# Kernel tuning notes

Measured on AMD Instinct MI355X. Metric: run time of the kernel, lower is better.

The kernel has to match this reference:

```python
import jax, jax.numpy as jnp
import numpy as np

N, E, F_IN, HID, HEADS, B = 50000, 800000, 128, 128, 2, 256
EPS = 1e-5
NEG_SLOPE = 0.2


def gat_conv(x, src, dst, W, a_src, a_dst, b, heads, out_c, concat):
    n = x.shape[0]
    h = (x @ W).reshape(n, heads, out_c)            # [N,H,C]
    alpha_src = jnp.sum(h * a_src, axis=-1)          # [N,H]
    alpha_dst = jnp.sum(h * a_dst, axis=-1)          # [N,H]
    e = jax.nn.leaky_relu(alpha_src[src] + alpha_dst[dst], NEG_SLOPE)  # [E2,H]
    # segment softmax over incoming edges per destination node
    emax = jax.ops.segment_max(e, dst, num_segments=n)
    ex = jnp.exp(e - emax[dst])
    denom = jax.ops.segment_sum(ex, dst, num_segments=n)
    alpha = ex / denom[dst]                          # [E2,H]
    msg = h[src] * alpha[:, :, None]                 # [E2,H,C]
    out = jax.ops.segment_sum(msg, dst, num_segments=n)  # [N,H,C]
    if concat:
        out = out.reshape(n, heads * out_c)
    else:
        out = out.mean(axis=1)
    return out + b


def batchnorm_eval(x, gamma, beta, mean, var):
    return gamma * (x - mean) * jax.lax.rsqrt(var + EPS) + beta


def setup_inputs() -> dict:
    key = jax.random.key(0)
    ks = jax.random.split(key, 16)
    x = jax.random.normal(ks[0], (N, F_IN), dtype=jnp.float32)
    edge_index = jax.random.randint(ks[1], (2, E), 0, N, dtype=jnp.int64)
    batch = (jnp.arange(N, dtype=jnp.int64) * B) // N  # sorted, every graph non-empty
    s1 = 1.0 / np.sqrt(F_IN)
    s2 = 1.0 / np.sqrt(HEADS * HID)
    return {
        "x": x,
        "edge_index": edge_index,
        "batch": batch,
        "W1": jax.random.normal(ks[2], (F_IN, HEADS * HID), dtype=jnp.float32) * s1,
        "a_src1": jax.random.normal(ks[3], (HEADS, HID), dtype=jnp.float32) * s1,
        "a_dst1": jax.random.normal(ks[4], (HEADS, HID), dtype=jnp.float32) * s1,
        "b1": jnp.zeros((HEADS * HID,), dtype=jnp.float32),
        "gamma1": jnp.ones((HEADS * HID,), dtype=jnp.float32),
        "beta1": jnp.zeros((HEADS * HID,), dtype=jnp.float32),
        "rm1": jax.random.normal(ks[5], (HEADS * HID,), dtype=jnp.float32) * 0.1,
        "rv1": jax.random.uniform(ks[6], (HEADS * HID,), dtype=jnp.float32, minval=0.5, maxval=1.5),
        "W2": jax.random.normal(ks[7], (HEADS * HID, HID), dtype=jnp.float32) * s2,
        "a_src2": jax.random.normal(ks[8], (1, HID), dtype=jnp.float32) * s2,
        "a_dst2": jax.random.normal(ks[9], (1, HID), dtype=jnp.float32) * s2,
        "b2": jnp.zeros((HID,), dtype=jnp.float32),
        "gamma2": jnp.ones((HID,), dtype=jnp.float32),
        "beta2": jnp.zeros((HID,), dtype=jnp.float32),
        "rm2": jax.random.normal(ks[10], (HID,), dtype=jnp.float32) * 0.1,
        "rv2": jax.random.uniform(ks[11], (HID,), dtype=jnp.float32, minval=0.5, maxval=1.5),
    }


def reference(x, edge_index, batch, W1, a_src1, a_dst1, b1, gamma1, beta1, rm1, rv1,
              W2, a_src2, a_dst2, b2, gamma2, beta2, rm2, rv2):
    n = x.shape[0]
    # PyG GATConv adds self-loops by default
    loops = jnp.arange(n, dtype=edge_index.dtype)
    src = jnp.concatenate([edge_index[0], loops])
    dst = jnp.concatenate([edge_index[1], loops])

    h = gat_conv(x, src, dst, W1, a_src1, a_dst1, b1, HEADS, HID, concat=True)
    h = jax.nn.relu(batchnorm_eval(h, gamma1, beta1, rm1, rv1))  # dropout = identity (eval)

    h = gat_conv(h, src, dst, W2, a_src2, a_dst2, b2, 1, HID, concat=False)
    h = jax.nn.relu(batchnorm_eval(h, gamma2, beta2, rm2, rv2))

    # global max pool over graphs
    h_D = jax.ops.segment_max(h, batch, num_segments=B)  # [B, HID]
    return h_D
```

## Files before the change

### kernel.cpp

```cpp
#include <hip/hip_runtime.h>
#include <hip/hip_bf16.h>
#include <math.h>

#define NEG_SLOPE 0.2f
#define EPSBN 1e-5f

typedef __attribute__((ext_vector_type(8))) short bf16x8;
typedef __attribute__((ext_vector_type(4))) float f32x4;

__device__ __forceinline__ float bfu2f(unsigned u_lo16) { return __uint_as_float(u_lo16 << 16); }
__device__ __forceinline__ unsigned short f2bf(float f) {
    return __bfloat16_as_ushort(__float2bfloat16(f));
}
__device__ __forceinline__ void splitf(float v, unsigned short &h, unsigned short &l) {
    __hip_bfloat16 hb = __float2bfloat16(v);
    float r = v - __bfloat162float(hb);
    h = __bfloat16_as_ushort(hb);
    l = __bfloat16_as_ushort(__float2bfloat16(r));
}

__global__ __launch_bounds__(256) void precompute_v(
    const float* __restrict__ W1, const float* __restrict__ as1,
    const float* __restrict__ ad1, float* __restrict__ vsd)
{
    int idx = blockIdx.x * 256 + threadIdx.x;
    if (idx >= 512) return;
    int k = idx & 127, which = idx >> 7;
    const float* av = ((which >= 2) ? ad1 : as1) + ((which & 1) ? 128 : 0);
    const float* wr = W1 + (size_t)k * 256 + ((which & 1) ? 128 : 0);
    float v = 0.f;
    for (int c = 0; c < 128; ++c) v += wr[c] * av[c];
    vsd[which * 128 + k] = v;
}

__global__ __launch_bounds__(256) void prep(
    const float* __restrict__ X, const float* __restrict__ vsd,
    const float* __restrict__ W1, const float* __restrict__ W2,
    const int* __restrict__ ei,
    unsigned short* __restrict__ Xh, float* __restrict__ asrc, float* __restrict__ adst,
    unsigned short* __restrict__ w1th, unsigned short* __restrict__ w1tl,
    unsigned short* __restrict__ w2th, unsigned short* __restrict__ w2tl,
    int* __restrict__ counts, int* __restrict__ erank,
    int Nn, int E, int nwB, int countB)
{
    const int b = blockIdx.x;
    const int tid = threadIdx.x;
    if (b < nwB) {
        int n = (int)((b * 256 + tid) >> 6);
        int lane = tid & 63;
        if (n >= Nn) return;
        float2 xv = *(const float2*)(X + (size_t)n * 128 + lane * 2);
        unsigned short hh[2] = {f2bf(xv.x), f2bf(xv.y)};
        *(unsigned*)(Xh + (size_t)n * 128 + lane * 2) = *(unsigned*)hh;
        int k = lane * 2;
        float p0 = xv.x * vsd[k]       + xv.y * vsd[k + 1];
        float p1 = xv.x * vsd[128 + k] + xv.y * vsd[129 + k];
        float p2 = xv.x * vsd[256 + k] + xv.y * vsd[257 + k];
        float p3 = xv.x * vsd[384 + k] + xv.y * vsd[385 + k];
        for (int off = 32; off; off >>= 1) {
            p0 += __shfl_xor(p0, off); p1 += __shfl_xor(p1, off);
            p2 += __shfl_xor(p2, off); p3 += __shfl_xor(p3, off);
        }
        if (lane == 0) {
            asrc[n * 2] = p0; asrc[n * 2 + 1] = p1;
            adst[n * 2] = p2; adst[n * 2 + 1] = p3;
        }
    } else if (b < nwB + countB) {
        int base = (b - nwB) * 2048 + tid;
        int E2 = E + Nn;
#pragma unroll
        for (int k = 0; k < 8; ++k) {
            int e = base + k * 256;
            if (e < E2) {
                int dst = (e < E) ? ei[E + e] : (e - E);
                erank[e] = atomicAdd(&counts[dst], 1);
            }
        }
    } else {
        int idx = (b - nwB - countB) * 256 + tid;
        if (idx < 32768) {
            int nn = idx >> 7, k = idx & 127;
            unsigned short h, l; splitf(W1[(size_t)k * 256 + nn], h, l);
            w1th[idx] = h; w1tl[idx] = l;
        } else if (idx < 65536) {
            int j = idx - 32768;
            int nn = j >> 8, k = j & 255;
            unsigned short h, l; splitf(W2[(size_t)k * 128 + nn], h, l);
            w2th[j] = h; w2tl[j] = l;
        }
    }
}

__global__ __launch_bounds__(256) void scan_block(
    const int* __restrict__ counts, int* __restrict__ offs, int* __restrict__ bsum, int Nn)
{
    __shared__ int s[256];
    int i = blockIdx.x * 256 + threadIdx.x;
    int v = (i < Nn) ? counts[i] : 0;
    s[threadIdx.x] = v;
    __syncthreads();
    for (int off = 1; off < 256; off <<= 1) {
        int t = (threadIdx.x >= off) ? s[threadIdx.x - off] : 0;
        __syncthreads();
        s[threadIdx.x] += t;
        __syncthreads();
    }
    if (i < Nn) offs[i] = s[threadIdx.x] - v;
    if (threadIdx.x == 255) bsum[blockIdx.x] = s[255];
}

__global__ __launch_bounds__(256) void finalize_offsets(
    const int* __restrict__ bsum, int* __restrict__ offs, int Nn, int E2)
{
    __shared__ int ws[4];
    int b = blockIdx.x, t = threadIdx.x;
    int v = (t < b) ? bsum[t] : 0;
    for (int off = 32; off; off >>= 1) v += __shfl_xor(v, off);
    if ((t & 63) == 0) ws[t >> 6] = v;
    __syncthreads();
    int S = ws[0] + ws[1] + ws[2] + ws[3];
    int i = b * 256 + t;
    if (i < Nn) offs[i] += S;
    if (b == 0 && t == 0) offs[Nn] = E2;
}

__global__ __launch_bounds__(256) void fill_edges(
    const int* __restrict__ ei, int E, int Nn,
    const int* __restrict__ offs, const int* __restrict__ erank,
    int* __restrict__ esrc)
{
    int base = blockIdx.x * 1024 + threadIdx.x;
    int E2 = E + Nn;
#pragma unroll
    for (int k = 0; k < 4; ++k) {
        int e = base + k * 256;
        if (e >= E2) continue;
        int src, dst;
        if (e < E) { src = ei[e]; dst = ei[E + e]; }
        else       { src = e - E; dst = e - E; }
        esrc[offs[dst] + erank[e]] = src;
    }
}

__device__ __forceinline__ void fma8(float wA, uint4 hv, float acc[8])
{
    acc[0] = fmaf(wA, bfu2f(hv.x & 0xffff), acc[0]);
    acc[1] = fmaf(wA, __uint_as_float(hv.x & 0xffff0000u), acc[1]);
    acc[2] = fmaf(wA, bfu2f(hv.y & 0xffff), acc[2]);
    acc[3] = fmaf(wA, __uint_as_float(hv.y & 0xffff0000u), acc[3]);
    acc[4] = fmaf(wA, bfu2f(hv.z & 0xffff), acc[4]);
    acc[5] = fmaf(wA, __uint_as_float(hv.z & 0xffff0000u), acc[5]);
    acc[6] = fmaf(wA, bfu2f(hv.w & 0xffff), acc[6]);
    acc[7] = fmaf(wA, __uint_as_float(hv.w & 0xffff0000u), acc[7]);
}

__device__ __forceinline__ void fma8x2(float wa, float wb, uint4 hv,
                                       float a0[8], float a1[8])
{
    float f;
    f = bfu2f(hv.x & 0xffff);                 a0[0]=fmaf(wa,f,a0[0]); a1[0]=fmaf(wb,f,a1[0]);
    f = __uint_as_float(hv.x & 0xffff0000u);  a0[1]=fmaf(wa,f,a0[1]); a1[1]=fmaf(wb,f,a1[1]);
    f = bfu2f(hv.y & 0xffff);                 a0[2]=fmaf(wa,f,a0[2]); a1[2]=fmaf(wb,f,a1[2]);
    f = __uint_as_float(hv.y & 0xffff0000u);  a0[3]=fmaf(wa,f,a0[3]); a1[3]=fmaf(wb,f,a1[3]);
    f = bfu2f(hv.z & 0xffff);                 a0[4]=fmaf(wa,f,a0[4]); a1[4]=fmaf(wb,f,a1[4]);
    f = __uint_as_float(hv.z & 0xffff0000u);  a0[5]=fmaf(wa,f,a0[5]); a1[5]=fmaf(wb,f,a1[5]);
    f = bfu2f(hv.w & 0xffff);                 a0[6]=fmaf(wa,f,a0[6]); a1[6]=fmaf(wb,f,a1[6]);
    f = __uint_as_float(hv.w & 0xffff0000u);  a0[7]=fmaf(wa,f,a0[7]); a1[7]=fmaf(wb,f,a1[7]);
}

__device__ __forceinline__ void gather1h(
    int sj, float w, int nc, int sub,
    const char* __restrict__ hb_c, float acc[8])
{
    for (int t = 0; t < nc; t += 4) {
        int e = t + sub;
        int sA = __shfl(sj, e);
        float wA = __shfl(w, e);
        uint4 hv = *(const uint4*)(hb_c + sA * 256);
        fma8(wA, hv, acc);
    }
}

__device__ __forceinline__ void gatherx(
    int sj, float w0, float w1, int nc, int sub,
    const char* __restrict__ hb_c, float a0[8], float a1[8])
{
    for (int t = 0; t < nc; t += 4) {
        int e = t + sub;
        int sA = __shfl(sj, e);
        float wa = __shfl(w0, e);
        float wb = __shfl(w1, e);
        uint4 hv = *(const uint4*)(hb_c + sA * 256);
        fma8x2(wa, wb, hv, a0, a1);
    }
}

__global__ __launch_bounds__(256) void spmm_x(
    const unsigned short* __restrict__ xh, const float* __restrict__ asrc,
    const float* __restrict__ adst, const int* __restrict__ offs,
    const int* __restrict__ esrc,
    unsigned short* __restrict__ xth, int Nn)
{
    int d = (int)((blockIdx.x * blockDim.x + threadIdx.x) >> 6);
    int lane = threadIdx.x & 63;
    if (d >= Nn) return;
    int beg = offs[d], end = offs[d + 1];
    int deg = end - beg;
    float ad0 = adst[d * 2], ad1 = adst[d * 2 + 1];
    const int sub = lane >> 4;
    const int cgrp = lane & 15;
    const char* hb_c = (const char*)xh + cgrp * 16;
    float a0[8] = {}, a1[8] = {};

    if (deg <= 64) {
        int sj = 0; float e0 = -1e30f, e1 = -1e30f;
        if (lane < deg) {
            sj = esrc[beg + lane];
            float2 av = *(const float2*)(asrc + (size_t)sj * 2);
            e0 = av.x + ad0; e0 = e0 > 0.f ? e0 : NEG_SLOPE * e0;
            e1 = av.y + ad1; e1 = e1 > 0.f ? e1 : NEG_SLOPE * e1;
        }
        float m0 = e0, m1 = e1;
        for (int off = 32; off; off >>= 1) {
            m0 = fmaxf(m0, __shfl_xor(m0, off));
            m1 = fmaxf(m1, __shfl_xor(m1, off));
        }
        float p0 = (lane < deg) ? expf(e0 - m0) : 0.f;
        float p1 = (lane < deg) ? expf(e1 - m1) : 0.f;
        float s0 = p0, s1 = p1;
        for (int off = 32; off; off >>= 1) {
            s0 += __shfl_xor(s0, off);
            s1 += __shfl_xor(s1, off);
        }
        float w0 = p0 * (1.f / s0), w1 = p1 * (1.f / s1);
        gatherx(sj, w0, w1, deg, sub, hb_c, a0, a1);
    } else {
        float m0 = -1e30f, m1 = -1e30f;
        for (int j = beg + lane; j < end; j += 64) {
            int s = esrc[j];
            float2 av = *(const float2*)(asrc + (size_t)s * 2);
            float e0 = av.x + ad0; e0 = e0 > 0.f ? e0 : NEG_SLOPE * e0;
            float e1 = av.y + ad1; e1 = e1 > 0.f ? e1 : NEG_SLOPE * e1;
            m0 = fmaxf(m0, e0); m1 = fmaxf(m1, e1);
        }
        for (int off = 32; off; off >>= 1) {
            m0 = fmaxf(m0, __shfl_xor(m0, off));
            m1 = fmaxf(m1, __shfl_xor(m1, off));
        }
        float s0 = 0.f, s1 = 0.f;
        for (int j = beg + lane; j < end; j += 64) {
            int s = esrc[j];
            float2 av = *(const float2*)(asrc + (size_t)s * 2);
            float e0 = av.x + ad0; e0 = e0 > 0.f ? e0 : NEG_SLOPE * e0;
            float e1 = av.y + ad1; e1 = e1 > 0.f ? e1 : NEG_SLOPE * e1;
            s0 += expf(e0 - m0); s1 += expf(e1 - m1);
        }
        for (int off = 32; off; off >>= 1) {
            s0 += __shfl_xor(s0, off);
            s1 += __shfl_xor(s1, off);
        }
        float rd0 = 1.f / s0, rd1 = 1.f / s1;
        for (int base = beg; base < end; base += 64) {
            int nc = end - base; if (nc > 64) nc = 64;
            int sj = 0; float w0 = 0.f, w1 = 0.f;
            if (lane < nc) {
                sj = esrc[base + lane];
                float2 av = *(const float2*)(asrc + (size_t)sj * 2);
                float e0 = av.x + ad0; e0 = e0 > 0.f ? e0 : NEG_SLOPE * e0;
                float e1 = av.y + ad1; e1 = e1 > 0.f ? e1 : NEG_SLOPE * e1;
                w0 = expf(e0 - m0) * rd0;
                w1 = expf(e1 - m1) * rd1;
            }
            gatherx(sj, w0, w1, nc, sub, hb_c, a0, a1);
        }
    }
#pragma unroll
    for (int i = 0; i < 8; ++i) {
        a0[i] += __shfl_xor(a0[i], 32); a0[i] += __shfl_xor(a0[i], 16);
        a1[i] += __shfl_xor(a1[i], 32); a1[i] += __shfl_xor(a1[i], 16);
    }
    if (lane < 16) {
        int cl = cgrp * 8;
        unsigned short h0[8], h1[8];
#pragma unroll
        for (int i = 0; i < 8; ++i) { h0[i] = f2bf(a0[i]); h1[i] = f2bf(a1[i]); }
        size_t rb = (size_t)d * 256;
        *(uint4*)(xth + rb + cl)       = *(uint4*)&h0[0];
        *(uint4*)(xth + rb + 128 + cl) = *(uint4*)&h1[0];
    }
}

__global__ __launch_bounds__(256) void gemm_bn_split(
    const unsigned short* __restrict__ Ah,
    const unsigned short* __restrict__ Bth, const unsigned short* __restrict__ Btl,
    const float* __restrict__ bias, const float* __restrict__ gamma,
    const float* __restrict__ beta, const float* __restrict__ rm,
    const float* __restrict__ rv,
    unsigned short* __restrict__ Ch, int M)
{
    __shared__ unsigned short smem[3][128][32];
    const int tid = threadIdx.x;
    const int lane = tid & 63;
    const int wave = tid >> 6;
    const int fr = lane & 15, g = lane >> 4;
    const int wr = (wave >> 1) * 64, wc = (wave & 1) * 64;
    const int rowBase = blockIdx.x * 128, colBase = blockIdx.y * 128;

    f32x4 acc[4][4] = {};

    for (int kk = 0; kk < 128; kk += 32) {
#pragma unroll
        for (int i = 0; i < 2; ++i) {
            int idx = tid + 256 * i;
            int r = idx >> 2, c = (idx & 3) * 8;
            int grow = rowBase + r;
            uint4 va_h = make_uint4(0, 0, 0, 0);
            if (grow < M) va_h = *(const uint4*)(Ah + (size_t)grow * 256 + colBase + kk + c);
            *(uint4*)&smem[0][r][c] = va_h;
            int gcol = colBase + r;
            *(uint4*)&smem[1][r][c] = *(const uint4*)(Bth + (size_t)gcol * 128 + kk + c);
            *(uint4*)&smem[2][r][c] = *(const uint4*)(Btl + (size_t)gcol * 128 + kk + c);
        }
        __syncthreads();

        bf16x8 ah[4], bh[4], bl[4];
#pragma unroll
        for (int m = 0; m < 4; ++m)
            ah[m] = *(const bf16x8*)&smem[0][wr + m * 16 + fr][g * 8];
#pragma unroll
        for (int n = 0; n < 4; ++n) {
            bh[n] = *(const bf16x8*)&smem[1][wc + n * 16 + fr][g * 8];
            bl[n] = *(const bf16x8*)&smem[2][wc + n * 16 + fr][g * 8];
        }
#pragma unroll
        for (int m = 0; m < 4; ++m)
#pragma unroll
            for (int n = 0; n < 4; ++n) {
                acc[m][n] = __builtin_amdgcn_mfma_f32_16x16x32_bf16(ah[m], bh[n], acc[m][n], 0, 0, 0);
                acc[m][n] = __builtin_amdgcn_mfma_f32_16x16x32_bf16(ah[m], bl[n], acc[m][n], 0, 0, 0);
            }
        __syncthreads();
    }

    {
        float bi[4], ga[4], bb[4], mu[4], iv[4];
#pragma unroll
        for (int n = 0; n < 4; ++n) {
            int c = colBase + wc + n * 16 + fr;
            bi[n] = bias[c]; ga[n] = gamma[c]; bb[n] = beta[c];
            mu[n] = rm[c];   iv[n] = rsqrtf(rv[c] + EPSBN);
        }
#pragma unroll
        for (int m = 0; m < 4; ++m)
#pragma unroll
            for (int n = 0; n < 4; ++n)
#pragma unroll
                for (int j = 0; j < 4; ++j) {
                    float v = acc[m][n][j] + bi[n];
                    v = ga[n] * (v - mu[n]) * iv[n] + bb[n];
                    acc[m][n][j] = fmaxf(v, 0.f);
                }
    }

    float* Cs = (float*)&smem[0][0][0];
    const int rl_w = (wr >> 6) * 16;
#pragma unroll
    for (int m = 0; m < 4; ++m) {
        __syncthreads();
#pragma unroll
        for (int n = 0; n < 4; ++n)
#pragma unroll
            for (int j = 0; j < 4; ++j)
                Cs[(rl_w + g * 4 + j) * 132 + wc + n * 16 + fr] = acc[m][n][j];
        __syncthreads();
        int rl = tid >> 3, c16 = (tid & 7) * 16;
        int grow = rowBase + (rl >> 4) * 64 + m * 16 + (rl & 15);
        if (grow < M) {
            unsigned short th[16];
#pragma unroll
            for (int i = 0; i < 16; ++i) th[i] = f2bf(Cs[rl * 132 + c16 + i]);
            size_t ob = (size_t)grow * 256 + colBase + c16;
            *(uint4*)(Ch + ob)     = *(uint4*)&th[0];
            *(uint4*)(Ch + ob + 8) = *(uint4*)&th[8];
        }
    }
}

__global__ __launch_bounds__(256) void gemm_bf16_attn(
    const unsigned short* __restrict__ Ah,
    const unsigned short* __restrict__ Bth, const unsigned short* __restrict__ Btl,
    unsigned short* __restrict__ Cb,
    const float* __restrict__ aSrc, const float* __restrict__ aDst,
    float* __restrict__ asrcOut, float* __restrict__ adstOut, int M)
{
    __shared__ unsigned short smem[3][128][32];
    const int tid = threadIdx.x;
    const int lane = tid & 63;
    const int wave = tid >> 6;
    const int fr = lane & 15, g = lane >> 4;
    const int wr = (wave >> 1) * 64, wc = (wave & 1) * 64;
    const int rowBase = blockIdx.x * 128;

    f32x4 acc[4][4] = {};

    for (int kk = 0; kk < 256; kk += 32) {
#pragma unroll
        for (int i = 0; i < 2; ++i) {
            int idx = tid + 256 * i;
            int r = idx >> 2, c = (idx & 3) * 8;
            int grow = rowBase + r;
            uint4 va_h = make_uint4(0, 0, 0, 0);
            if (grow < M) va_h = *(const uint4*)(Ah + (size_t)grow * 256 + kk + c);
            *(uint4*)&smem[0][r][c] = va_h;
            *(uint4*)&smem[1][r][c] = *(const uint4*)(Bth + (size_t)r * 256 + kk + c);
            *(uint4*)&smem[2][r][c] = *(const uint4*)(Btl + (size_t)r * 256 + kk + c);
        }
        __syncthreads();

        bf16x8 ah[4], bh[4], bl[4];
#pragma unroll
        for (int m = 0; m < 4; ++m)
            ah[m] = *(const bf16x8*)&smem[0][wr + m * 16 + fr][g * 8];
#pragma unroll
        for (int n = 0; n < 4; ++n) {
            bh[n] = *(const bf16x8*)&smem[1][wc + n * 16 + fr][g * 8];
            bl[n] = *(const bf16x8*)&smem[2][wc + n * 16 + fr][g * 8];
        }
#pragma unroll
        for (int m = 0; m < 4; ++m)
#pragma unroll
            for (int n = 0; n < 4; ++n) {
                acc[m][n] = __builtin_amdgcn_mfma_f32_16x16x32_bf16(ah[m], bh[n], acc[m][n], 0, 0, 0);
                acc[m][n] = __builtin_amdgcn_mfma_f32_16x16x32_bf16(ah[m], bl[n], acc[m][n], 0, 0, 0);
            }
        __syncthreads();
    }

    {
        float avs[4], avd[4];
#pragma unroll
        for (int n = 0; n < 4; ++n) {
            int col = wc + n * 16 + fr;
            avs[n] = aSrc[col]; avd[n] = aDst[col];
        }
#pragma unroll
        for (int m = 0; m < 4; ++m) {
            float ps[4], pd[4];
#pragma unroll
            for (int j = 0; j < 4; ++j) {
                ps[j] = acc[m][0][j] * avs[0] + acc[m][1][j] * avs[1]
                      + acc[m][2][j] * avs[2] + acc[m][3][j] * avs[3];
                pd[j] = acc[m][0][j] * avd[0] + acc[m][1][j] * avd[1]
                      + acc[m][2][j] * avd[2] + acc[m][3][j] * avd[3];
            }
#pragma unroll
            for (int off = 8; off; off >>= 1)
#pragma unroll
                for (int j = 0; j < 4; ++j) {
                    ps[j] += __shfl_xor(ps[j], off);
                    pd[j] += __shfl_xor(pd[j], off);
                }
            if (fr == 0) {
#pragma unroll
                for (int j = 0; j < 4; ++j) {
                    int grow = rowBase + wr + m * 16 + g * 4 + j;
                    if (grow < M) {
                        atomicAdd(asrcOut + grow, ps[j]);
                        atomicAdd(adstOut + grow, pd[j]);
                    }
                }
            }
        }
    }

    float* Cs = (float*)&smem[0][0][0];
    const int rl_w = (wr >> 6) * 16;
#pragma unroll
    for (int m = 0; m < 4; ++m) {
        __syncthreads();
#pragma unroll
        for (int n = 0; n < 4; ++n)
#pragma unroll
            for (int j = 0; j < 4; ++j)
                Cs[(rl_w + g * 4 + j) * 132 + wc + n * 16 + fr] = acc[m][n][j];
        __syncthreads();
        int rl = tid >> 3, c16 = (tid & 7) * 16;
        int grow = rowBase + (rl >> 4) * 64 + m * 16 + (rl & 15);
        if (grow < M) {
            unsigned short tmp[16];
#pragma unroll
            for (int i = 0; i < 16; ++i) tmp[i] = f2bf(Cs[rl * 132 + c16 + i]);
            *(uint4*)(Cb + (size_t)grow * 128 + c16)     = *(uint4*)&tmp[0];
            *(uint4*)(Cb + (size_t)grow * 128 + c16 + 8) = *(uint4*)&tmp[8];
        }
    }
}

__global__ __launch_bounds__(256) void spmm2(
    const unsigned short* __restrict__ h2b, const float* __restrict__ asrc,
    const float* __restrict__ adst, const int* __restrict__ offs,
    const int* __restrict__ esrc,
    const float* __restrict__ b2, const float* __restrict__ gamma,
    const float* __restrict__ beta, const float* __restrict__ rm,
    const float* __restrict__ rv, unsigned short* __restrict__ x3b, int Nn)
{
    int d = (int)((blockIdx.x * blockDim.x + threadIdx.x) >> 6);
    int lane = threadIdx.x & 63;
    if (d >= Nn) return;
    int beg = offs[d], end = offs[d + 1];
    int deg = end - beg;
    float ad = adst[d];
    const int sub = lane >> 4;
    const int cgrp = lane & 15;
    const char* hb_c = (const char*)h2b + cgrp * 16;
    float acc[8] = {};

    if (deg <= 64) {
        int sj = 0; float ev = -1e30f;
        if (lane < deg) {
            sj = esrc[beg + lane];
            float e = asrc[sj] + ad; ev = e > 0.f ? e : NEG_SLOPE * e;
        }
        float m = ev;
        for (int off = 32; off; off >>= 1) m = fmaxf(m, __shfl_xor(m, off));
        float p = (lane < deg) ? expf(ev - m) : 0.f;
        float s = p;
        for (int off = 32; off; off >>= 1) s += __shfl_xor(s, off);
        float w = p * (1.f / s);
        gather1h(sj, w, deg, sub, hb_c, acc);
    } else {
        float m = -1e30f;
        for (int j = beg + lane; j < end; j += 64) {
            int s = esrc[j];
            float e = asrc[s] + ad; e = e > 0.f ? e : NEG_SLOPE * e;
            m = fmaxf(m, e);
        }
        for (int off = 32; off; off >>= 1) m = fmaxf(m, __shfl_xor(m, off));
        float sd = 0.f;
        for (int j = beg + lane; j < end; j += 64) {
            int s = esrc[j];
            float e = asrc[s] + ad; e = e > 0.f ? e : NEG_SLOPE * e;
            sd += expf(e - m);
        }
        for (int off = 32; off; off >>= 1) sd += __shfl_xor(sd, off);
        float rd = 1.f / sd;
        for (int base = beg; base < end; base += 64) {
            int nc = end - base; if (nc > 64) nc = 64;
            int sj = 0; float wj = 0.f;
            if (lane < nc) {
                sj = esrc[base + lane];
                float e = asrc[sj] + ad; e = e > 0.f ? e : NEG_SLOPE * e;
                wj = expf(e - m) * rd;
            }
            gather1h(sj, wj, nc, sub, hb_c, acc);
        }
    }
#pragma unroll
    for (int i = 0; i < 8; ++i) {
        acc[i] += __shfl_xor(acc[i], 32);
        acc[i] += __shfl_xor(acc[i], 16);
    }
    if (lane < 16) {
        int cl = cgrp * 8;
        unsigned short hh[8];
#pragma unroll
        for (int i = 0; i < 8; ++i) {
            int c = cl + i;
            float v = acc[i] + b2[c];
            v = gamma[c] * (v - rm[c]) * rsqrtf(rv[c] + EPSBN) + beta[c];
            hh[i] = f2bf(fmaxf(v, 0.f));
        }
        *(uint4*)(x3b + (size_t)d * 128 + cl) = *(uint4*)&hh[0];
    }
}

__global__ __launch_bounds__(128) void pool_max_graph(
    const unsigned short* __restrict__ x3b, const int* __restrict__ bat,
    float* __restrict__ out, int Nn)
{
    int g = blockIdx.x;
    int c = threadIdx.x;
    int lo = 0, hi = Nn;
    while (lo < hi) { int mid = (lo + hi) >> 1; if (bat[mid] < g) lo = mid + 1; else hi = mid; }
    int beg = lo;
    hi = Nn;
    while (lo < hi) { int mid = (lo + hi) >> 1; if (bat[mid] < g + 1) lo = mid + 1; else hi = mid; }
    int end = lo;
    float acc = -1e30f;
    for (int n = beg; n < end; ++n)
        acc = fmaxf(acc, bfu2f((unsigned)x3b[(size_t)n * 128 + c]));
    out[(size_t)g * 128 + c] = acc;
}

extern "C" void kernel_launch(void* const* d_in, const int* in_sizes, int n_in,
                              void* d_out, int out_size, void* d_ws, size_t ws_size,
                              hipStream_t stream)
{
    const float* x   = (const float*)d_in[0];
    const int*   ei  = (const int*)d_in[1];
    const int*   bat = (const int*)d_in[2];
    const float* W1  = (const float*)d_in[3];
    const float* as1 = (const float*)d_in[4];
    const float* ad1 = (const float*)d_in[5];
    const float* b1  = (const float*)d_in[6];
    const float* g1  = (const float*)d_in[7];
    const float* be1 = (const float*)d_in[8];
    const float* rm1 = (const float*)d_in[9];
    const float* rv1 = (const float*)d_in[10];
    const float* W2  = (const float*)d_in[11];
    const float* as2 = (const float*)d_in[12];
    const float* ad2 = (const float*)d_in[13];
    const float* b2  = (const float*)d_in[14];
    const float* g2  = (const float*)d_in[15];
    const float* be2 = (const float*)d_in[16];
    const float* rm2 = (const float*)d_in[17];
    const float* rv2 = (const float*)d_in[18];
    float* out = (float*)d_out;

    const int Nn = in_sizes[0] / 128;
    const int E  = in_sizes[1] / 2;
    const int E2 = E + Nn;
    const int B  = out_size / 128;

    char* p = (char*)d_ws;
    size_t off = 0;
    auto alloc = [&](size_t bytes) -> void* {
        void* r = p + off;
        off = (off + bytes + 255) & ~(size_t)255;
        return r;
    };
    unsigned short* xh    = (unsigned short*)alloc((size_t)Nn * 128 * 2);
    unsigned short* w1th  = (unsigned short*)alloc(256 * 128 * 2);
    unsigned short* w1tl  = (unsigned short*)alloc(256 * 128 * 2);
    unsigned short* w2th  = (unsigned short*)alloc(128 * 256 * 2);
    unsigned short* w2tl  = (unsigned short*)alloc(128 * 256 * 2);
    unsigned short* xth   = (unsigned short*)alloc((size_t)Nn * 256 * 2);
    unsigned short* x2h   = (unsigned short*)alloc((size_t)Nn * 256 * 2);
    float*          vsd   = (float*)alloc(4 * 128 * 4);
    float*          asrc1 = (float*)alloc((size_t)Nn * 2 * 4);
    float*          adst1 = (float*)alloc((size_t)Nn * 2 * 4);
    float*          attnv = (float*)alloc((size_t)Nn * 2 * 4);
    float*          asrc2 = attnv;
    float*          adst2 = attnv + Nn;
    int*            counts= (int*)alloc((size_t)Nn * 4);
    int*            erank = (int*)alloc((size_t)E2 * 4);
    int*            offs  = (int*)alloc((size_t)(Nn + 1) * 4);
    int*            bsum  = (int*)alloc(256 * 4);
    int*            esrc  = (int*)alloc((size_t)E2 * 4);
    unsigned short* x3b   = xth;
    unsigned short* h2b   = xh;

    const int nb = (Nn + 255) / 256;
    const int nwB = (Nn + 3) / 4;
    const int countB = (E2 + 2047) / 2048;
    const int gmB = (Nn + 127) / 128;

    hipMemsetAsync(counts, 0, (size_t)Nn * 4, stream);
    hipMemsetAsync(attnv, 0, (size_t)Nn * 2 * 4, stream);

    precompute_v<<<2, 256, 0, stream>>>(W1, as1, ad1, vsd);
    prep<<<nwB + countB + 256, 256, 0, stream>>>(
        x, vsd, W1, W2, ei, xh, asrc1, adst1,
        w1th, w1tl, w2th, w2tl, counts, erank, Nn, E, nwB, countB);

    scan_block<<<nb, 256, 0, stream>>>(counts, offs, bsum, Nn);
    finalize_offsets<<<nb, 256, 0, stream>>>(bsum, offs, Nn, E2);
    fill_edges<<<(E2 + 1023) / 1024, 256, 0, stream>>>(ei, E, Nn, offs, erank, esrc);

    spmm_x<<<nwB, 256, 0, stream>>>(xh, asrc1, adst1, offs, esrc, xth, Nn);
    gemm_bn_split<<<dim3(gmB, 2), 256, 0, stream>>>(
        xth, w1th, w1tl, b1, g1, be1, rm1, rv1, x2h, Nn);

    gemm_bf16_attn<<<gmB, 256, 0, stream>>>(
        x2h, w2th, w2tl, h2b, as2, ad2, asrc2, adst2, Nn);
    spmm2<<<nwB, 256, 0, stream>>>(h2b, asrc2, adst2, offs, esrc,
                                   b2, g2, be2, rm2, rv2, x3b, Nn);

    pool_max_graph<<<B, 128, 0, stream>>>(x3b, bat, out, Nn);
}
```

Before: 246.4 us.

## Replicate per-node edge counters to spread atomic contention in CSR build

Edge counting now atomically increments one of eight replicated counter arrays, chosen by edge index, so concurrent atomics on the same destination are spread across copies. The scan kernel turns each node's replica counts into per-replica prefix offsets, and fill_edges adds that replica offset when placing each edge. The count blocks are reordered to launch first and now handle one edge per thread. The cost is an eight-fold larger counter memset and eight reads plus eight writes per node in the scan.

```diff
diff --git a/kernel.cpp b/kernel.cpp
--- a/kernel.cpp
+++ b/kernel.cpp
@@ -4,6 +4,7 @@
 
 #define NEG_SLOPE 0.2f
 #define EPSBN 1e-5f
+#define NREP 8
 
 typedef __attribute__((ext_vector_type(8))) short bf16x8;
 typedef __attribute__((ext_vector_type(4))) float f32x4;
@@ -45,8 +46,14 @@
 {
     const int b = blockIdx.x;
     const int tid = threadIdx.x;
-    if (b < nwB) {
-        int n = (int)((b * 256 + tid) >> 6);
+    if (b < countB) {
+        int e = b * 256 + tid;
+        int E2 = E + Nn;
+        if (e >= E2) return;
+        int dst = (e < E) ? ei[E + e] : (e - E);
+        erank[e] = atomicAdd(&counts[(e & (NREP - 1)) * Nn + dst], 1);
+    } else if (b < countB + nwB) {
+        int n = (int)(((b - countB) * 256 + tid) >> 6);
         int lane = tid & 63;
         if (n >= Nn) return;
         float2 xv = *(const float2*)(X + (size_t)n * 128 + lane * 2);
@@ -65,19 +72,8 @@
             asrc[n * 2] = p0; asrc[n * 2 + 1] = p1;
             adst[n * 2] = p2; adst[n * 2 + 1] = p3;
         }
-    } else if (b < nwB + countB) {
-        int base = (b - nwB) * 2048 + tid;
-        int E2 = E + Nn;
-#pragma unroll
-        for (int k = 0; k < 8; ++k) {
-            int e = base + k * 256;
-            if (e < E2) {
-                int dst = (e < E) ? ei[E + e] : (e - E);
-                erank[e] = atomicAdd(&counts[dst], 1);
-            }
-        }
     } else {
-        int idx = (b - nwB - countB) * 256 + tid;
+        int idx = (b - countB - nwB) * 256 + tid;
         if (idx < 32768) {
             int nn = idx >> 7, k = idx & 127;
             unsigned short h, l; splitf(W1[(size_t)k * 256 + nn], h, l);
@@ -92,11 +88,20 @@
 }
 
 __global__ __launch_bounds__(256) void scan_block(
-    const int* __restrict__ counts, int* __restrict__ offs, int* __restrict__ bsum, int Nn)
+    int* __restrict__ counts, int* __restrict__ offs, int* __restrict__ bsum, int Nn)
 {
     __shared__ int s[256];
     int i = blockIdx.x * 256 + threadIdx.x;
-    int v = (i < Nn) ? counts[i] : 0;
+    int v = 0;
+    if (i < Nn) {
+        int c[NREP];
+#pragma unroll
+        for (int r = 0; r < NREP; ++r) c[r] = counts[r * Nn + i];
+        int run = 0;
+#pragma unroll
+        for (int r = 0; r < NREP; ++r) { counts[r * Nn + i] = run; run += c[r]; }
+        v = run;
+    }
     s[threadIdx.x] = v;
     __syncthreads();
     for (int off = 1; off < 256; off <<= 1) {
@@ -124,22 +129,18 @@
     if (b == 0 && t == 0) offs[Nn] = E2;
 }
 
-__global__ __launch_bounds__(256) void fill_edges(
+__global__ void fill_edges(
     const int* __restrict__ ei, int E, int Nn,
-    const int* __restrict__ offs, const int* __restrict__ erank,
-    int* __restrict__ esrc)
-{
-    int base = blockIdx.x * 1024 + threadIdx.x;
+    const int* __restrict__ offs, const int* __restrict__ repoff,
+    const int* __restrict__ erank, int* __restrict__ esrc)
+{
+    int e = blockIdx.x * blockDim.x + threadIdx.x;
     int E2 = E + Nn;
-#pragma unroll
-    for (int k = 0; k < 4; ++k) {
-        int e = base + k * 256;
-        if (e >= E2) continue;
-        int src, dst;
-        if (e < E) { src = ei[e]; dst = ei[E + e]; }
-        else       { src = e - E; dst = e - E; }
-        esrc[offs[dst] + erank[e]] = src;
-    }
+    if (e >= E2) return;
+    int src, dst;
+    if (e < E) { src = ei[e]; dst = ei[E + e]; }
+    else       { src = e - E; dst = e - E; }
+    esrc[offs[dst] + repoff[(e & (NREP - 1)) * Nn + dst] + erank[e]] = src;
 }
 
 __device__ __forceinline__ void fma8(float wA, uint4 hv, float acc[8])
@@ -642,7 +643,7 @@
     float*          attnv = (float*)alloc((size_t)Nn * 2 * 4);
     float*          asrc2 = attnv;
     float*          adst2 = attnv + Nn;
-    int*            counts= (int*)alloc((size_t)Nn * 4);
+    int*            counts= (int*)alloc((size_t)NREP * Nn * 4);
     int*            erank = (int*)alloc((size_t)E2 * 4);
     int*            offs  = (int*)alloc((size_t)(Nn + 1) * 4);
     int*            bsum  = (int*)alloc(256 * 4);
@@ -652,20 +653,20 @@
 
     const int nb = (Nn + 255) / 256;
     const int nwB = (Nn + 3) / 4;
-    const int countB = (E2 + 2047) / 2048;
+    const int countB = (E2 + 255) / 256;
     const int gmB = (Nn + 127) / 128;
 
-    hipMemsetAsync(counts, 0, (size_t)Nn * 4, stream);
+    hipMemsetAsync(counts, 0, (size_t)NREP * Nn * 4, stream);
     hipMemsetAsync(attnv, 0, (size_t)Nn * 2 * 4, stream);
 
     precompute_v<<<2, 256, 0, stream>>>(W1, as1, ad1, vsd);
-    prep<<<nwB + countB + 256, 256, 0, stream>>>(
+    prep<<<countB + nwB + 256, 256, 0, stream>>>(
         x, vsd, W1, W2, ei, xh, asrc1, adst1,
         w1th, w1tl, w2th, w2tl, counts, erank, Nn, E, nwB, countB);
 
     scan_block<<<nb, 256, 0, stream>>>(counts, offs, bsum, Nn);
     finalize_offsets<<<nb, 256, 0, stream>>>(bsum, offs, Nn, E2);
-    fill_edges<<<(E2 + 1023) / 1024, 256, 0, stream>>>(ei, E, Nn, offs, erank, esrc);
+    fill_edges<<<(E2 + 255) / 256, 256, 0, stream>>>(ei, E, Nn, offs, counts, erank, esrc);
 
     spmm_x<<<nwB, 256, 0, stream>>>(xh, asrc1, adst1, offs, esrc, xth, Nn);
     gemm_bn_split<<<dim3(gmB, 2), 256, 0, stream>>>(
```

New measurement: 246.0 us. No clear change (-0.2%).
